# Kernel tuning notes

Measured on AMD Instinct MI355X. Metric: run time of the kernel, lower is better.

Reference implementation:

```python
import jax, jax.numpy as jnp
import numpy as np

D_MODEL = 1024
HEADS = 16
HEAD_DIM = D_MODEL // HEADS


def setup_inputs() -> dict:
    key = jax.random.key(0)
    ks = jax.random.split(key, 6)
    B, S, D = 2, 2048, D_MODEL
    scale = 1.0 / np.sqrt(D)
    x = jax.random.normal(ks[0], (B, S, D), dtype=jnp.float32)
    mask = jax.random.randint(ks[1], (B, S), 0, 2, dtype=jnp.int32)
    Wq = jax.random.normal(ks[2], (D, D), dtype=jnp.float32) * scale
    Wk = jax.random.normal(ks[3], (D, D), dtype=jnp.float32) * scale
    Wv = jax.random.normal(ks[4], (D, D), dtype=jnp.float32) * scale
    Wp = jax.random.normal(ks[5], (D, D), dtype=jnp.float32) * scale
    zb = jnp.zeros((D,), dtype=jnp.float32)
    return {"x": x, "mask": mask, "Wq": Wq, "bq": zb, "Wk": Wk, "bk": zb,
            "Wv": Wv, "bv": zb, "Wp": Wp, "bp": zb}


def reference(x, mask, Wq, bq, Wk, bk, Wv, bv, Wp, bp):
    B, S, D = x.shape
    H, Dh = HEADS, HEAD_DIM

    def split_heads(t):  # [B,S,D] -> [B,H,S,Dh]
        return t.reshape(B, S, H, Dh).transpose(0, 2, 1, 3)

    q = split_heads(x @ Wq + bq)
    k = split_heads(x @ Wk + bk)
    v = split_heads(x @ Wv + bv)

    att = jnp.einsum('bhqd,bhkd->bhqk', q, k) / jnp.sqrt(jnp.float32(Dh))
    # key-padding mask: [B,S] -> [B,1,1,S]; masked positions -> -inf
    m = (mask[:, None, None, :] != 0)
    att = jnp.where(m, att, -jnp.inf)
    att = jax.nn.softmax(att, axis=-1)
    # rows that were fully masked produce NaN -> zero them (masked_fill(isnan, 0))
    att = jnp.where(jnp.isnan(att), 0.0, att)

    y = jnp.einsum('bhqk,bhkd->bhqd', att, v)  # [B,H,S,Dh]
    y = y.transpose(0, 2, 1, 3).reshape(B, S, D)
    return y @ Wp + bp
```

## Files before the change

### kernel.cpp

```cpp
#include <hip/hip_runtime.h>
#include <math.h>

#define D_MODEL 1024
#define HEADS 16
#define HEAD_DIM 64
#define SEQ 2048
#define BATCH 2
#define KVT 64
#define QTILE 64
#define SCALE_Q 0.18033688f

typedef __attribute__((ext_vector_type(8))) short bf16x8;
typedef __attribute__((ext_vector_type(4))) float f32x4;

__device__ __forceinline__ short f2bf(float f) {
    union { float f; unsigned u; } v; v.f = f;
    unsigned r = (v.u + 0x7FFFu + ((v.u >> 16) & 1u)) >> 16;
    return (short)r;
}

__device__ __forceinline__ unsigned cvt_pk_bf16(float lo, float hi) {
    unsigned r;
    asm("v_cvt_pk_bf16_f32 %0, %1, %2" : "=v"(r) : "v"(lo), "v"(hi));
    return r;
}

__device__ __forceinline__ float fexp2(float x) {
    float r;
    asm("v_exp_f32 %0, %1" : "=v"(r) : "v"(x));
    return r;
}

__global__ __launch_bounds__(256) void prep(
    const float* __restrict__ x, const float* __restrict__ Wq,
    const float* __restrict__ Wk, const float* __restrict__ Wv,
    const float* __restrict__ Wp, const int* __restrict__ mask,
    short* __restrict__ xb, short* __restrict__ Wqkvt,
    short* __restrict__ Wpt, float* __restrict__ maskf) {
    __shared__ float t[32][33];
    const int bid = blockIdx.x;
    if (bid < 2048) {
        const int i = bid * 256 + threadIdx.x;
        float4 a = ((const float4*)x)[2 * i];
        float4 b = ((const float4*)x)[2 * i + 1];
        short r[8] = {f2bf(a.x), f2bf(a.y), f2bf(a.z), f2bf(a.w),
                      f2bf(b.x), f2bf(b.y), f2bf(b.z), f2bf(b.w)};
        *(uint4*)(xb + 8 * i) = *(uint4*)r;
    } else if (bid < 6144) {
        const int tt = bid - 2048;
        const int z = tt >> 10;
        const int rem = tt & 1023;
        const float* W = z == 0 ? Wq : z == 1 ? Wk : z == 2 ? Wv : Wp;
        short* dst = (z < 3) ? Wqkvt + (size_t)z * 1024 * 1024 : Wpt;
        const int n0 = (rem & 31) * 32, k0 = (rem >> 5) * 32;
        const int tx = threadIdx.x & 31, ty = threadIdx.x >> 5;
#pragma unroll
        for (int j = 0; j < 4; ++j)
            t[ty + j * 8][tx] = W[(size_t)(k0 + ty + j * 8) * 1024 + n0 + tx];
        __syncthreads();
#pragma unroll
        for (int j = 0; j < 4; ++j) {
            const int n = ty + j * 8;
            dst[(size_t)(n0 + n) * 1024 + k0 + tx] = f2bf(t[tx][n]);
        }
    } else {
        const int i = (bid - 6144) * 256 + threadIdx.x;
        maskf[i] = mask[i] ? 0.f : -INFINITY;
    }
}

template <int MODE>
__global__ __launch_bounds__(256) void mfma_gemm(
    const short* __restrict__ A, const short* __restrict__ Bt,
    const float* __restrict__ b0, const float* __restrict__ b1,
    const float* __restrict__ b2, float* __restrict__ outf,
    short* __restrict__ o0, short* __restrict__ o1, short* __restrict__ o2,
    int M, int N, int K) {
    __shared__ short As[2 * 128 * 32];
    __shared__ short Bs[2 * 128 * 32];

    const int tid = threadIdx.x;
    const int wave = tid >> 6, lane = tid & 63;
    const int l15 = lane & 15, lhi = lane >> 4;
    const int wm = wave >> 1, wn = wave & 1;
    const int bm0 = blockIdx.y * 128, bn0 = blockIdx.x * 128;

    f32x4 acc[4][4];
#pragma unroll
    for (int m = 0; m < 4; ++m)
#pragma unroll
        for (int n = 0; n < 4; ++n) acc[m][n] = (f32x4){0.f, 0.f, 0.f, 0.f};

#define STAGE_G(buf, kt_)                                                         \
    {                                                                             \
        const int k0 = (kt_) * 32;                                                \
        _Pragma("unroll") for (int p = 0; p < 2; ++p) {                           \
            const int o = (wave * 2 + p) * 64 + lane;                             \
            const int r = o >> 2;                                                 \
            const int gs = (o & 3) ^ ((r >> 1) & 3);                              \
            __builtin_amdgcn_global_load_lds(                                     \
                (const __attribute__((address_space(1))) void*)(                  \
                    A + (size_t)(bm0 + r) * K + k0 + gs * 8),                     \
                (__attribute__((address_space(3))) void*)(                        \
                    As + (size_t)(buf) * 4096 + (wave * 2 + p) * 512),            \
                16, 0, 0);                                                        \
            __builtin_amdgcn_global_load_lds(                                     \
                (const __attribute__((address_space(1))) void*)(                  \
                    Bt + (size_t)(bn0 + r) * K + k0 + gs * 8),                    \
                (__attribute__((address_space(3))) void*)(                        \
                    Bs + (size_t)(buf) * 4096 + (wave * 2 + p) * 512),            \
                16, 0, 0);                                                        \
        }                                                                         \
    }

    const int NT = K / 32;
    STAGE_G(0, 0);
    __syncthreads();
    for (int kt = 0; kt < NT; ++kt) {
        const int cur = kt & 1;
        if (kt + 1 < NT) STAGE_G((kt + 1) & 1, kt + 1);
        bf16x8 af[4], bf[4];
        const int sg = (lhi ^ ((l15 >> 1) & 3)) * 16;
#pragma unroll
        for (int m = 0; m < 4; ++m)
            af[m] = *(const bf16x8*)((char*)As + cur * 8192 +
                                     (wm * 64 + m * 16 + l15) * 64 + sg);
#pragma unroll
        for (int n = 0; n < 4; ++n)
            bf[n] = *(const bf16x8*)((char*)Bs + cur * 8192 +
                                     (wn * 64 + n * 16 + l15) * 64 + sg);
        __builtin_amdgcn_s_setprio(1);
#pragma unroll
        for (int m = 0; m < 4; ++m)
#pragma unroll
            for (int n = 0; n < 4; ++n)
                acc[m][n] = __builtin_amdgcn_mfma_f32_16x16x32_bf16(af[m], bf[n], acc[m][n], 0, 0, 0);
        __builtin_amdgcn_s_setprio(0);
        __syncthreads();
    }
#undef STAGE_G

    const int which = (MODE == 1) ? (bn0 >> 10) : 0;
#pragma unroll
    for (int m = 0; m < 4; ++m) {
#pragma unroll
        for (int n = 0; n < 4; ++n) {
            const int col = bn0 + wn * 64 + n * 16 + l15;
            if (MODE == 0) {
#pragma unroll
                for (int rr = 0; rr < 4; ++rr) {
                    const int row = bm0 + wm * 64 + m * 16 + lhi * 4 + rr;
                    outf[(size_t)row * N + col] = acc[m][n][rr] + b0[col];
                }
            } else {
                const int cc = col & 1023;
                const int h = cc >> 6, dh = cc & 63;
                const int row0 = bm0 + wm * 64 + m * 16 + lhi * 4;
                const int b = row0 >> 11, s0 = row0 & (SEQ - 1);
                if (which == 2) {
                    const float bias = b2[cc];
                    uint2 w;
                    w.x = cvt_pk_bf16(acc[m][n][0] + bias, acc[m][n][1] + bias);
                    w.y = cvt_pk_bf16(acc[m][n][2] + bias, acc[m][n][3] + bias);
                    *(uint2*)(o2 + ((size_t)(b * HEADS + h) * HEAD_DIM + dh) * SEQ + s0) = w;
                } else {
                    const float bias = (which == 0 ? b0 : b1)[cc];
                    short* dst = which == 0 ? o0 : o1;
#pragma unroll
                    for (int rr = 0; rr < 4; ++rr) {
                        float v = acc[m][n][rr] + bias;
                        if (which == 0) v *= SCALE_Q;
                        dst[(((size_t)(b * HEADS + h)) * SEQ + s0 + rr) * HEAD_DIM + dh] = f2bf(v);
                    }
                }
            }
        }
    }
}

__global__ __launch_bounds__(256, 4) void flash_attn(
    const short* __restrict__ Q, const short* __restrict__ K,
    const short* __restrict__ Vt, const float* __restrict__ maskf,
    short* __restrict__ Y) {
    __shared__ unsigned char kt[2][KVT * 128];
    __shared__ unsigned char vt[2][HEAD_DIM * 128];
    __shared__ unsigned char pb[4][16 * 128];

    const int tid = threadIdx.x;
    const int wave = tid >> 6;
    const int lane = tid & 63;
    const int l15 = lane & 15;
    const int lhi = lane >> 4;

    const int nwg = gridDim.x;
    const int wg = blockIdx.x;
    const int swz = (wg & 7) * (nwg >> 3) + (wg >> 3);
    const int qt = swz & 31;
    const int bh = swz >> 5;
    const int b = bh >> 4;

    const int q0 = qt * QTILE + wave * 16;

    const short* Qp = Q + ((size_t)bh * SEQ + q0 + l15) * HEAD_DIM;
    bf16x8 qf[2];
    qf[0] = *(const bf16x8*)(Qp + 8 * lhi);
    qf[1] = *(const bf16x8*)(Qp + 8 * lhi + 32);

    const unsigned char* Kb8 = (const unsigned char*)(K + (size_t)bh * SEQ * HEAD_DIM);
    const unsigned char* Vb8 = (const unsigned char*)(Vt + (size_t)bh * HEAD_DIM * SEQ);
    const float* mb = maskf + b * SEQ;

#define STAGE(buf, kvi)                                                            \
    {                                                                              \
        const unsigned char* kbase = Kb8 + (size_t)(kvi) * KVT * 128;              \
        const unsigned char* vbase = Vb8 + (size_t)(kvi) * 128;                    \
        _Pragma("unroll") for (int p = 0; p < 2; ++p) {                            \
            const int o = (wave * 2 + p) * 64 + lane;                              \
            const int row = o >> 3;                                                \
            const int inner = (o & 7) * 16;                                        \
            const int src = inner ^ ((row & 7) << 4);                              \
            __builtin_amdgcn_global_load_lds(                                      \
                (const __attribute__((address_space(1))) void*)(                   \
                    kbase + row * 128 + src),                                      \
                (__attribute__((address_space(3))) void*)(                         \
                    &kt[buf][(wave * 2 + p) * 1024]),                              \
                16, 0, 0);                                                         \
            __builtin_amdgcn_global_load_lds(                                      \
                (const __attribute__((address_space(1))) void*)(                   \
                    vbase + (size_t)row * (SEQ * 2) + src),                        \
                (__attribute__((address_space(3))) void*)(                         \
                    &vt[buf][(wave * 2 + p) * 1024]),                              \
                16, 0, 0);                                                         \
        }                                                                          \
    }

    f32x4 accO[4];
    float mrow = -30000.f, lrow = 0.f;
#pragma unroll
    for (int i = 0; i < 4; ++i) accO[i] = (f32x4){0.f, 0.f, 0.f, 0.f};

    STAGE(0, 0);
    __syncthreads();

    for (int kv = 0; kv < SEQ / KVT; ++kv) {
        const int cur = kv & 1;
        if (kv + 1 < SEQ / KVT) STAGE((kv + 1) & 1, kv + 1);

        const int k0 = kv * KVT;

        f32x4 accS[4];
#pragma unroll
        for (int nt = 0; nt < 4; ++nt) accS[nt] = (f32x4){0.f, 0.f, 0.f, 0.f};
#pragma unroll
        for (int c = 0; c < 2; ++c) {
            bf16x8 kf[4];
#pragma unroll
            for (int nt = 0; nt < 4; ++nt) {
                const int key = l15 + 16 * nt;
                kf[nt] = *(const bf16x8*)(kt[cur] + key * 128 +
                                          ((16 * lhi + 64 * c) ^ ((key & 7) << 4)));
            }
            __builtin_amdgcn_s_setprio(1);
#pragma unroll
            for (int nt = 0; nt < 4; ++nt)
                accS[nt] = __builtin_amdgcn_mfma_f32_16x16x32_bf16(kf[nt], qf[c], accS[nt], 0, 0, 0);
            __builtin_amdgcn_s_setprio(0);
        }

#pragma unroll
        for (int nt = 0; nt < 4; ++nt) {
            const f32x4 ma = *(const f32x4*)(mb + k0 + 16 * nt + 4 * lhi);
#pragma unroll
            for (int r = 0; r < 4; ++r) accS[nt][r] += ma[r];
        }

        float t0 = fmaxf(fmaxf(accS[0][0], accS[0][1]), fmaxf(accS[0][2], accS[0][3]));
        float t1 = fmaxf(fmaxf(accS[1][0], accS[1][1]), fmaxf(accS[1][2], accS[1][3]));
        float t2 = fmaxf(fmaxf(accS[2][0], accS[2][1]), fmaxf(accS[2][2], accS[2][3]));
        float t3 = fmaxf(fmaxf(accS[3][0], accS[3][1]), fmaxf(accS[3][2], accS[3][3]));
        float smax = fmaxf(fmaxf(t0, t1), fmaxf(t2, t3));
        smax = fmaxf(smax, __shfl_xor(smax, 16));
        smax = fmaxf(smax, __shfl_xor(smax, 32));

        if (!__all(smax <= mrow + 11.5f)) {
            const float mn = fmaxf(mrow, smax);
            const float alpha = fexp2(mrow - mn);
            lrow *= alpha;
#pragma unroll
            for (int d = 0; d < 4; ++d)
#pragma unroll
                for (int r = 0; r < 4; ++r) accO[d][r] *= alpha;
            mrow = mn;
        }

        float rs = 0.f;
#pragma unroll
        for (int nt = 0; nt < 4; ++nt)
#pragma unroll
            for (int r = 0; r < 4; ++r) {
                const float pv = fexp2(accS[nt][r] - mrow);
                accS[nt][r] = pv;
                rs += pv;
            }
        rs += __shfl_xor(rs, 16);
        rs += __shfl_xor(rs, 32);
        lrow += rs;

#pragma unroll
        for (int nt = 0; nt < 4; ++nt) {
            uint2 w;
            w.x = cvt_pk_bf16(accS[nt][0], accS[nt][1]);
            w.y = cvt_pk_bf16(accS[nt][2], accS[nt][3]);
            *(uint2*)(pb[wave] + l15 * 128 + ((32 * nt + 8 * lhi) ^ (l15 << 3))) = w;
        }

#pragma unroll
        for (int c = 0; c < 2; ++c) {
            union { bf16x8 v; uint2 u[2]; } pfu;
            pfu.u[0] = *(const uint2*)(pb[wave] + l15 * 128 +
                                       ((16 * lhi + 64 * c) ^ (l15 << 3)));
            pfu.u[1] = *(const uint2*)(pb[wave] + l15 * 128 +
                                       ((16 * lhi + 64 * c + 8) ^ (l15 << 3)));
            const bf16x8 pf = pfu.v;
            bf16x8 vf[4];
#pragma unroll
            for (int d = 0; d < 4; ++d) {
                const int dh = l15 + 16 * d;
                vf[d] = *(const bf16x8*)(vt[cur] + dh * 128 +
                                         ((16 * lhi + 64 * c) ^ ((dh & 7) << 4)));
            }
            __builtin_amdgcn_s_setprio(1);
#pragma unroll
            for (int d = 0; d < 4; ++d)
                accO[d] = __builtin_amdgcn_mfma_f32_16x16x32_bf16(vf[d], pf, accO[d], 0, 0, 0);
            __builtin_amdgcn_s_setprio(0);
        }
        __syncthreads();
    }
#undef STAGE

    const float inv = (lrow > 0.f) ? 1.f / lrow : 0.f;
    const int qg = q0 + l15;
    short* Yp = Y + ((size_t)b * SEQ + qg) * D_MODEL + (bh & 15) * HEAD_DIM;
#pragma unroll
    for (int d = 0; d < 4; ++d) {
        uint2 w;
        w.x = cvt_pk_bf16(accO[d][0] * inv, accO[d][1] * inv);
        w.y = cvt_pk_bf16(accO[d][2] * inv, accO[d][3] * inv);
        *(uint2*)(Yp + 16 * d + 4 * lhi) = w;
    }
}

extern "C" void kernel_launch(void* const* d_in, const int* in_sizes, int n_in,
                              void* d_out, int out_size, void* d_ws, size_t ws_size,
                              hipStream_t stream) {
    const float* x    = (const float*)d_in[0];
    const int*   mask = (const int*)  d_in[1];
    const float* Wq   = (const float*)d_in[2];
    const float* bq   = (const float*)d_in[3];
    const float* Wk   = (const float*)d_in[4];
    const float* bk   = (const float*)d_in[5];
    const float* Wv   = (const float*)d_in[6];
    const float* bv   = (const float*)d_in[7];
    const float* Wp   = (const float*)d_in[8];
    const float* bp   = (const float*)d_in[9];
    float* out = (float*)d_out;

    short* ws    = (short*)d_ws;
    short* xb    = ws;
    short* Wqkvt = xb + ((size_t)4 << 20);
    short* Wpt   = Wqkvt + ((size_t)3 << 20);
    short* Qb    = Wpt + ((size_t)1 << 20);
    short* Kb    = Qb + ((size_t)4 << 20);
    short* Vtb   = Kb + ((size_t)4 << 20);
    short* Yb    = Vtb + ((size_t)4 << 20);
    float* maskf = (float*)(Yb + ((size_t)4 << 20));

    const int M = BATCH * SEQ;

    prep<<<dim3(6160), 256, 0, stream>>>(x, Wq, Wk, Wv, Wp, mask,
                                         xb, Wqkvt, Wpt, maskf);

    mfma_gemm<1><<<dim3(3 * D_MODEL / 128, M / 128), 256, 0, stream>>>(
        xb, Wqkvt, bq, bk, bv, nullptr, Qb, Kb, Vtb, M, 3 * D_MODEL, D_MODEL);

    flash_attn<<<dim3(BATCH * HEADS * (SEQ / QTILE)), 256, 0, stream>>>(Qb, Kb, Vtb, maskf, Yb);

    mfma_gemm<0><<<dim3(D_MODEL / 128, M / 128), 256, 0, stream>>>(
        Yb, Wpt, bp, bp, bp, out, nullptr, nullptr, nullptr, M, D_MODEL, D_MODEL);
}
```

Baseline: 135.2 us.

## Use 32x32x16 MFMA with 32 query rows per wave in flash attention

The attention kernel now gives each wave 32 query rows (128 per workgroup) instead of 16, and switches from 16x16x32 to 32x32x16 bf16 MFMA for both QK^T and PV. Each K/V tile staged in LDS is therefore reused across twice as many queries, which halves K/V traffic and halves the number of workgroups. Cross-lane reductions drop one shuffle step. In exchange it uses more registers, the launch bounds drop to 2 waves per EU, and the grid is smaller, so latency hiding and load balance may suffer.

Result: no change. 135.4 us (+0.2%).

```diff
diff --git a/kernel.cpp b/kernel.cpp
--- a/kernel.cpp
+++ b/kernel.cpp
@@ -7,11 +7,12 @@
 #define SEQ 2048
 #define BATCH 2
 #define KVT 64
-#define QTILE 64
+#define QTILE 128
 #define SCALE_Q 0.18033688f
 
 typedef __attribute__((ext_vector_type(8))) short bf16x8;
 typedef __attribute__((ext_vector_type(4))) float f32x4;
+typedef __attribute__((ext_vector_type(16))) float f32x16;
 
 __device__ __forceinline__ short f2bf(float f) {
     union { float f; unsigned u; } v; v.f = f;
@@ -178,33 +179,35 @@
     }
 }
 
-__global__ __launch_bounds__(256, 4) void flash_attn(
+__global__ __launch_bounds__(256, 2) void flash_attn(
     const short* __restrict__ Q, const short* __restrict__ K,
     const short* __restrict__ Vt, const float* __restrict__ maskf,
     short* __restrict__ Y) {
     __shared__ unsigned char kt[2][KVT * 128];
     __shared__ unsigned char vt[2][HEAD_DIM * 128];
-    __shared__ unsigned char pb[4][16 * 128];
+    __shared__ unsigned char pb[4][32 * 128];
 
     const int tid = threadIdx.x;
     const int wave = tid >> 6;
     const int lane = tid & 63;
-    const int l15 = lane & 15;
-    const int lhi = lane >> 4;
+    const int l31 = lane & 31;
+    const int lh = lane >> 5;
+    const int psw = (l31 & 7) << 4;
 
     const int nwg = gridDim.x;
     const int wg = blockIdx.x;
     const int swz = (wg & 7) * (nwg >> 3) + (wg >> 3);
-    const int qt = swz & 31;
-    const int bh = swz >> 5;
+    const int qt = swz & 15;
+    const int bh = swz >> 4;
     const int b = bh >> 4;
 
-    const int q0 = qt * QTILE + wave * 16;
-
-    const short* Qp = Q + ((size_t)bh * SEQ + q0 + l15) * HEAD_DIM;
-    bf16x8 qf[2];
-    qf[0] = *(const bf16x8*)(Qp + 8 * lhi);
-    qf[1] = *(const bf16x8*)(Qp + 8 * lhi + 32);
+    const int q0 = qt * QTILE + wave * 32;
+
+    const short* Qp = Q + ((size_t)bh * SEQ + q0 + l31) * HEAD_DIM;
+    bf16x8 qf[4];
+#pragma unroll
+    for (int s = 0; s < 4; ++s)
+        qf[s] = *(const bf16x8*)(Qp + 16 * s + 8 * lh);
 
     const unsigned char* Kb8 = (const unsigned char*)(K + (size_t)bh * SEQ * HEAD_DIM);
     const unsigned char* Vb8 = (const unsigned char*)(Vt + (size_t)bh * HEAD_DIM * SEQ);
@@ -234,10 +237,12 @@
         }                                                                          \
     }
 
-    f32x4 accO[4];
+    f32x16 accO[2];
     float mrow = -30000.f, lrow = 0.f;
 #pragma unroll
-    for (int i = 0; i < 4; ++i) accO[i] = (f32x4){0.f, 0.f, 0.f, 0.f};
+    for (int d = 0; d < 2; ++d)
+#pragma unroll
+        for (int r = 0; r < 16; ++r) accO[d][r] = 0.f;
 
     STAGE(0, 0);
     __syncthreads();
@@ -248,38 +253,46 @@
 
         const int k0 = kv * KVT;
 
-        f32x4 accS[4];
-#pragma unroll
-        for (int nt = 0; nt < 4; ++nt) accS[nt] = (f32x4){0.f, 0.f, 0.f, 0.f};
-#pragma unroll
-        for (int c = 0; c < 2; ++c) {
-            bf16x8 kf[4];
-#pragma unroll
-            for (int nt = 0; nt < 4; ++nt) {
-                const int key = l15 + 16 * nt;
-                kf[nt] = *(const bf16x8*)(kt[cur] + key * 128 +
-                                          ((16 * lhi + 64 * c) ^ ((key & 7) << 4)));
+        f32x16 accS[2];
+#pragma unroll
+        for (int kb = 0; kb < 2; ++kb)
+#pragma unroll
+            for (int r = 0; r < 16; ++r) accS[kb][r] = 0.f;
+#pragma unroll
+        for (int s = 0; s < 4; ++s) {
+            bf16x8 kf[2];
+#pragma unroll
+            for (int kb = 0; kb < 2; ++kb) {
+                const int row = 32 * kb + l31;
+                kf[kb] = *(const bf16x8*)(kt[cur] + row * 128 +
+                                          ((32 * s + 16 * lh) ^ ((row & 7) << 4)));
             }
             __builtin_amdgcn_s_setprio(1);
 #pragma unroll
-            for (int nt = 0; nt < 4; ++nt)
-                accS[nt] = __builtin_amdgcn_mfma_f32_16x16x32_bf16(kf[nt], qf[c], accS[nt], 0, 0, 0);
+            for (int kb = 0; kb < 2; ++kb)
+                accS[kb] = __builtin_amdgcn_mfma_f32_32x32x16_bf16(kf[kb], qf[s], accS[kb], 0, 0, 0);
             __builtin_amdgcn_s_setprio(0);
         }
 
 #pragma unroll
-        for (int nt = 0; nt < 4; ++nt) {
-            const f32x4 ma = *(const f32x4*)(mb + k0 + 16 * nt + 4 * lhi);
-#pragma unroll
-            for (int r = 0; r < 4; ++r) accS[nt][r] += ma[r];
-        }
-
-        float t0 = fmaxf(fmaxf(accS[0][0], accS[0][1]), fmaxf(accS[0][2], accS[0][3]));
-        float t1 = fmaxf(fmaxf(accS[1][0], accS[1][1]), fmaxf(accS[1][2], accS[1][3]));
-        float t2 = fmaxf(fmaxf(accS[2][0], accS[2][1]), fmaxf(accS[2][2], accS[2][3]));
-        float t3 = fmaxf(fmaxf(accS[3][0], accS[3][1]), fmaxf(accS[3][2], accS[3][3]));
-        float smax = fmaxf(fmaxf(t0, t1), fmaxf(t2, t3));
-        smax = fmaxf(smax, __shfl_xor(smax, 16));
+        for (int kb = 0; kb < 2; ++kb)
+#pragma unroll
+            for (int g = 0; g < 4; ++g) {
+                const f32x4 ma = *(const f32x4*)(mb + k0 + 32 * kb + 8 * g + 4 * lh);
+#pragma unroll
+                for (int j = 0; j < 4; ++j) accS[kb][4 * g + j] += ma[j];
+            }
+
+        float mx[2];
+#pragma unroll
+        for (int kb = 0; kb < 2; ++kb) {
+            float a0 = fmaxf(fmaxf(accS[kb][0], accS[kb][1]), fmaxf(accS[kb][2], accS[kb][3]));
+            float a1 = fmaxf(fmaxf(accS[kb][4], accS[kb][5]), fmaxf(accS[kb][6], accS[kb][7]));
+            float a2 = fmaxf(fmaxf(accS[kb][8], accS[kb][9]), fmaxf(accS[kb][10], accS[kb][11]));
+            float a3 = fmaxf(fmaxf(accS[kb][12], accS[kb][13]), fmaxf(accS[kb][14], accS[kb][15]));
+            mx[kb] = fmaxf(fmaxf(a0, a1), fmaxf(a2, a3));
+        }
+        float smax = fmaxf(mx[0], mx[1]);
         smax = fmaxf(smax, __shfl_xor(smax, 32));
 
         if (!__all(smax <= mrow + 11.5f)) {
@@ -287,68 +300,68 @@
             const float alpha = fexp2(mrow - mn);
             lrow *= alpha;
 #pragma unroll
-            for (int d = 0; d < 4; ++d)
-#pragma unroll
-                for (int r = 0; r < 4; ++r) accO[d][r] *= alpha;
+            for (int d = 0; d < 2; ++d)
+#pragma unroll
+                for (int r = 0; r < 16; ++r) accO[d][r] *= alpha;
             mrow = mn;
         }
 
         float rs = 0.f;
 #pragma unroll
-        for (int nt = 0; nt < 4; ++nt)
-#pragma unroll
-            for (int r = 0; r < 4; ++r) {
-                const float pv = fexp2(accS[nt][r] - mrow);
-                accS[nt][r] = pv;
+        for (int kb = 0; kb < 2; ++kb)
+#pragma unroll
+            for (int r = 0; r < 16; ++r) {
+                const float pv = fexp2(accS[kb][r] - mrow);
+                accS[kb][r] = pv;
                 rs += pv;
             }
-        rs += __shfl_xor(rs, 16);
         rs += __shfl_xor(rs, 32);
         lrow += rs;
 
 #pragma unroll
-        for (int nt = 0; nt < 4; ++nt) {
+        for (int kb = 0; kb < 2; ++kb)
+#pragma unroll
+            for (int g = 0; g < 4; ++g) {
+                uint2 w;
+                w.x = cvt_pk_bf16(accS[kb][4 * g], accS[kb][4 * g + 1]);
+                w.y = cvt_pk_bf16(accS[kb][4 * g + 2], accS[kb][4 * g + 3]);
+                *(uint2*)(pb[wave] + l31 * 128 +
+                          ((64 * kb + 16 * g + 8 * lh) ^ psw)) = w;
+            }
+
+#pragma unroll
+        for (int t = 0; t < 4; ++t) {
+            const bf16x8 pf = *(const bf16x8*)(pb[wave] + l31 * 128 +
+                                               ((32 * t + 16 * lh) ^ psw));
+            bf16x8 vf[2];
+#pragma unroll
+            for (int db = 0; db < 2; ++db) {
+                const int row = 32 * db + l31;
+                vf[db] = *(const bf16x8*)(vt[cur] + row * 128 +
+                                          ((32 * t + 16 * lh) ^ ((row & 7) << 4)));
+            }
+            __builtin_amdgcn_s_setprio(1);
+#pragma unroll
+            for (int db = 0; db < 2; ++db)
+                accO[db] = __builtin_amdgcn_mfma_f32_32x32x16_bf16(vf[db], pf, accO[db], 0, 0, 0);
+            __builtin_amdgcn_s_setprio(0);
+        }
+        __syncthreads();
+    }
+#undef STAGE
+
+    const float inv = (lrow > 0.f) ? 1.f / lrow : 0.f;
+    const int qg = q0 + l31;
+    short* Yp = Y + ((size_t)b * SEQ + qg) * D_MODEL + (bh & 15) * HEAD_DIM;
+#pragma unroll
+    for (int db = 0; db < 2; ++db)
+#pragma unroll
+        for (int g = 0; g < 4; ++g) {
             uint2 w;
-            w.x = cvt_pk_bf16(accS[nt][0], accS[nt][1]);
-            w.y = cvt_pk_bf16(accS[nt][2], accS[nt][3]);
-            *(uint2*)(pb[wave] + l15 * 128 + ((32 * nt + 8 * lhi) ^ (l15 << 3))) = w;
-        }
-
-#pragma unroll
-        for (int c = 0; c < 2; ++c) {
-            union { bf16x8 v; uint2 u[2]; } pfu;
-            pfu.u[0] = *(const uint2*)(pb[wave] + l15 * 128 +
-                                       ((16 * lhi + 64 * c) ^ (l15 << 3)));
-            pfu.u[1] = *(const uint2*)(pb[wave] + l15 * 128 +
-                                       ((16 * lhi + 64 * c + 8) ^ (l15 << 3)));
-            const bf16x8 pf = pfu.v;
-            bf16x8 vf[4];
-#pragma unroll
-            for (int d = 0; d < 4; ++d) {
-                const int dh = l15 + 16 * d;
-                vf[d] = *(const bf16x8*)(vt[cur] + dh * 128 +
-                                         ((16 * lhi + 64 * c) ^ ((dh & 7) << 4)));
-            }
-            __builtin_amdgcn_s_setprio(1);
-#pragma unroll
-            for (int d = 0; d < 4; ++d)
-                accO[d] = __builtin_amdgcn_mfma_f32_16x16x32_bf16(vf[d], pf, accO[d], 0, 0, 0);
-            __builtin_amdgcn_s_setprio(0);
-        }
-        __syncthreads();
-    }
-#undef STAGE
-
-    const float inv = (lrow > 0.f) ? 1.f / lrow : 0.f;
-    const int qg = q0 + l15;
-    short* Yp = Y + ((size_t)b * SEQ + qg) * D_MODEL + (bh & 15) * HEAD_DIM;
-#pragma unroll
-    for (int d = 0; d < 4; ++d) {
-        uint2 w;
-        w.x = cvt_pk_bf16(accO[d][0] * inv, accO[d][1] * inv);
-        w.y = cvt_pk_bf16(accO[d][2] * inv, accO[d][3] * inv);
-        *(uint2*)(Yp + 16 * d + 4 * lhi) = w;
-    }
+            w.x = cvt_pk_bf16(accO[db][4 * g] * inv, accO[db][4 * g + 1] * inv);
+            w.y = cvt_pk_bf16(accO[db][4 * g + 2] * inv, accO[db][4 * g + 3] * inv);
+            *(uint2*)(Yp + 32 * db + 8 * g + 4 * lh) = w;
+        }
 }
 
 extern "C" void kernel_launch(void* const* d_in, const int* in_sizes, int n_in,
```
